# Kernel optimization log

Hardware: AMD Instinct MI355X
Metric: run time of the kernel (lower is better)

## Reference

```python
import jax, jax.numpy as jnp
import numpy as np

PERIODS = [4, 2, 1]   # base_periods[:n_period]
TEMPERATURE = 0.1
TOPM = 20
EPS = 1e-12


def _l2norm(v, axis):
    n = jnp.sqrt(jnp.sum(v * v, axis=axis, keepdims=True))
    return v / jnp.maximum(n, EPS)


def decompose_mg(x):
    """x: [B, L, C] -> mg: [G, B, L, C] (offset removed, as in torch code)."""
    B, L, C = x.shape
    mg = []
    for g in PERIODS:
        cur = x.reshape(B, L // g, g, C).mean(axis=2)      # unfold(size=g, step=g).mean(-1)
        cur = jnp.repeat(cur, g, axis=1)                   # repeat_interleave back to L
        mg.append(cur)
    mg = jnp.stack(mg, axis=0)                             # [G, B, L, C]
    return mg - mg[:, :, -1:, :]                           # remove per-series last-step offset


def extract_channel_state(mg):
    """mg: [G, B, L, C] -> [G, B, C, 4] (mean, std, slope, mean |diff|)."""
    L = mg.shape[2]
    mean = mg.mean(axis=2)
    std = mg.std(axis=2)                                   # unbiased=False (ddof=0)
    slope = (mg[:, :, -1, :] - mg[:, :, 0, :]) / float(L - 1)
    abs_diff = jnp.abs(mg[:, :, 1:, :] - mg[:, :, :-1, :]).mean(axis=2)
    return jnp.stack([mean, std, slope, abs_diff], axis=-1)


def setup_inputs() -> dict:
    key = jax.random.key(0)
    k1, k2, k3 = jax.random.split(key, 3)
    B, L, C, G, T, P = 32, 512, 64, 3, 10000, 96
    x = jax.random.normal(k1, (B, L, C), dtype=jnp.float32)
    pool_state = jax.random.normal(k2, (G, T, C, 4), dtype=jnp.float32)
    y_pool = jax.random.normal(k3, (T, P, C), dtype=jnp.float32)
    return {"x": x, "pool_state": pool_state, "y_pool": y_pool}


def reference(x, pool_state, y_pool):
    # Multi-scale decomposition of query batch
    q_mg = decompose_mg(x)                                  # [G, B, L, C]
    q_state = extract_channel_state(q_mg)                   # [G, B, C, 4]
    # Normalized channel-state similarity vs candidate pool
    q = _l2norm(q_state, axis=-1)
    p = _l2norm(pool_state, axis=-1)
    sim = jnp.einsum('gbcd,gtcd->gbct', q, p)               # [G, B, C, T]
    sim = sim.mean(axis=0)                                  # combine granularities -> [B, C, T]
    # Top-m retrieval per (batch, channel)
    vals, idx = jax.lax.top_k(sim, TOPM)                    # [B, C, M]
    w = jax.nn.softmax(vals / TEMPERATURE, axis=-1)         # [B, C, M]
    # Gather retrieved future windows, channelwise: y_pool [T, P, C]
    C = y_pool.shape[2]
    y_ct = jnp.transpose(y_pool, (2, 0, 1))                 # [C, T, P]
    gathered = y_ct[jnp.arange(C)[None, :, None], idx]      # [B, C, M, P]
    out = jnp.einsum('bcm,bcmp->bpc', w, gathered)          # [B, P, C]
    return out
```

## Files before the change

### kernel.cpp

```cpp
#include <hip/hip_runtime.h>
#include <hip/hip_fp16.h>
#include <math.h>

#define NB 32
#define NL 512
#define NC 64
#define NG 3
#define NT 10000
#define NP 96
#define TOPM 20
#define M1 8
#define NCH 256
#define CHUNK 40
#define QK 16
#define NCAND 64
#define PNBLK 1250
#define NENT (NB * NC * TOPM)
#define BINCAP 64
#define P16STR ((size_t)NT * NC)

union H2U { uint2 u; __half2 h[2]; };

__global__ __launch_bounds__(512) void pre_kernel(const float* __restrict__ x,
                                                  const float* __restrict__ ps,
                                                  double* __restrict__ q,
                                                  uint2* __restrict__ phat16) {
  __shared__ double s_sum[8][3][64], s_sq[8][3][64], s_abs[8][3][64];
  __shared__ double s_first[3][64], s_last[3][64];
  if (blockIdx.x < NB) {
    const int b = blockIdx.x, w = threadIdx.x >> 6, c = threadIdx.x & 63;
    const float* xp = x + (size_t)b * NL * NC + c;
    const int l0 = w * 64;
    double sum[3] = {0, 0, 0}, sumsq[3] = {0, 0, 0}, sumabs[3] = {0, 0, 0};
    double prev[3] = {0, 0, 0}, first[3] = {0, 0, 0};
    if (w > 0) {
      double e0 = xp[(l0 - 4) * NC], e1 = xp[(l0 - 3) * NC];
      double e2 = xp[(l0 - 2) * NC], e3 = xp[(l0 - 1) * NC];
      prev[2] = e3; prev[1] = (e2 + e3) * 0.5; prev[0] = (e0 + e1 + e2 + e3) * 0.25;
    }
    double acc2 = 0.0, acc4 = 0.0;
    for (int i = 0; i < 64; ++i) {
      const int l = l0 + i;
      double v = (double)xp[l * NC];
      sum[2] += v; sumsq[2] += v * v;
      if (l == 0) first[2] = v; else sumabs[2] += fabs(v - prev[2]);
      prev[2] = v;
      acc2 += v;
      if (l & 1) {
        double cur = acc2 * 0.5; acc2 = 0.0;
        sum[1] += cur; sumsq[1] += cur * cur;
        if (l == 1) first[1] = cur; else sumabs[1] += fabs(cur - prev[1]);
        prev[1] = cur;
      }
      acc4 += v;
      if ((l & 3) == 3) {
        double cur = acc4 * 0.25; acc4 = 0.0;
        sum[0] += cur; sumsq[0] += cur * cur;
        if (l == 3) first[0] = cur; else sumabs[0] += fabs(cur - prev[0]);
        prev[0] = cur;
      }
    }
    for (int g = 0; g < 3; ++g) {
      s_sum[w][g][c] = sum[g]; s_sq[w][g][c] = sumsq[g]; s_abs[w][g][c] = sumabs[g];
    }
    if (w == 0) { for (int g = 0; g < 3; ++g) s_first[g][c] = first[g]; }
    if (w == 7) { for (int g = 0; g < 3; ++g) s_last[g][c] = prev[g]; }
    __syncthreads();
    if (w == 0) {
      const double J[3] = {128.0, 256.0, 512.0};
      for (int g = 0; g < 3; ++g) {
        double S = 0, Q2 = 0, A = 0;
        for (int ww = 0; ww < 8; ++ww) {
          S += s_sum[ww][g][c]; Q2 += s_sq[ww][g][c]; A += s_abs[ww][g][c];
        }
        double mean = S / J[g];
        double var = Q2 / J[g] - mean * mean; if (var < 0.0) var = 0.0;
        double last = s_last[g][c];
        double s0 = mean - last;
        double s1 = sqrt(var);
        double s2 = (last - s_first[g][c]) * (1.0 / 511.0);
        double s3 = A * (1.0 / 511.0);
        double n = sqrt(s0 * s0 + s1 * s1 + s2 * s2 + s3 * s3);
        double inv = 1.0 / fmax(n, 1e-12);
        double* qp = q + ((((size_t)g * NB) + b) * NC + c) * 4;
        qp[0] = s0 * inv; qp[1] = s1 * inv; qp[2] = s2 * inv; qp[3] = s3 * inv;
      }
    }
  } else {
    const int i = (blockIdx.x - NB) * 512 + threadIdx.x;
    if (i < NT * NC) {
#pragma unroll
      for (int g = 0; g < 3; ++g) {
        const size_t off = ((size_t)g * NT * NC + i) * 4;
        const float4 pv = *reinterpret_cast<const float4*>(ps + off);
        double p0 = pv.x, p1 = pv.y, p2 = pv.z, p3 = pv.w;
        double inv = 1.0 / fmax(sqrt(p0 * p0 + p1 * p1 + p2 * p2 + p3 * p3), 1e-12);
        H2U o;
        o.h[0] = __halves2half2(__float2half_rn((float)(p0 * inv)),
                                __float2half_rn((float)(p1 * inv)));
        o.h[1] = __halves2half2(__float2half_rn((float)(p2 * inv)),
                                __float2half_rn((float)(p3 * inv)));
        phat16[(size_t)g * P16STR + i] = o.u;
      }
    }
  }
}

__device__ __forceinline__ unsigned mkkey16(float v, int t) {
  unsigned h = (unsigned)__half_as_ushort(__float2half_rn(v));
  h = (h & 0x8000u) ? ((~h) & 0xFFFFu) : (h | 0x8000u);
  return (h << 16) | (0xFFFFu - (unsigned)t);
}

__device__ __forceinline__ void insert8k(unsigned k, unsigned key[M1]) {
  unsigned cv = k;
#pragma unroll
  for (int m = 0; m < M1; ++m) {
    bool sw = cv > key[m];
    unsigned tv = sw ? key[m] : cv;
    key[m] = sw ? cv : key[m];
    cv = tv;
  }
}

#if defined(__has_builtin)
#if __has_builtin(__builtin_amdgcn_fdot2)
#define HAVE_FDOT2 1
#endif
#endif

__device__ __forceinline__ float sim_dot(const uint2* __restrict__ p16,
                                         size_t o,
#ifdef HAVE_FDOT2
                                         const __half2 qh[6]
#else
                                         const float qv[12]
#endif
                                         ) {
  H2U a0, a1, a2;
  a0.u = p16[o];
  a1.u = p16[P16STR + o];
  a2.u = p16[2 * P16STR + o];
#ifdef HAVE_FDOT2
  float s = 0.f;
  s = __builtin_amdgcn_fdot2(qh[0], a0.h[0], s, false);
  s = __builtin_amdgcn_fdot2(qh[1], a0.h[1], s, false);
  s = __builtin_amdgcn_fdot2(qh[2], a1.h[0], s, false);
  s = __builtin_amdgcn_fdot2(qh[3], a1.h[1], s, false);
  s = __builtin_amdgcn_fdot2(qh[4], a2.h[0], s, false);
  s = __builtin_amdgcn_fdot2(qh[5], a2.h[1], s, false);
  return s;
#else
  float2 f0 = __half22float2(a0.h[0]), f1 = __half22float2(a0.h[1]);
  float2 f2 = __half22float2(a1.h[0]), f3 = __half22float2(a1.h[1]);
  float2 f4 = __half22float2(a2.h[0]), f5 = __half22float2(a2.h[1]);
  return qv[0] * f0.x + qv[1] * f0.y + qv[2] * f1.x + qv[3] * f1.y +
         qv[4] * f2.x + qv[5] * f2.y + qv[6] * f3.x + qv[7] * f3.y +
         qv[8] * f4.x + qv[9] * f4.y + qv[10] * f5.x + qv[11] * f5.y;
#endif
}

__global__ __launch_bounds__(1024, 8) void sim32_kernel(
    const uint2* __restrict__ p16, const double* __restrict__ q,
    unsigned* __restrict__ ckey, int* __restrict__ hist) {
  if (blockIdx.x == 0 && blockIdx.y < 10) {
    const int idx = blockIdx.y * 1024 + threadIdx.x;
    if (idx < NT) hist[idx] = 0;
  }
  const int wav = threadIdx.x >> 6;
  const int c = threadIdx.x & 63;
  const int b = blockIdx.x * 16 + wav;
  const int ch = blockIdx.y;
#ifdef HAVE_FDOT2
  __half2 qh[6];
#pragma unroll
  for (int g = 0; g < 3; ++g) {
    const double* qp = q + ((((size_t)g * NB) + b) * NC + c) * 4;
    qh[g * 2 + 0] = __halves2half2(__float2half_rn((float)(qp[0] * (1.0 / 3.0))),
                                   __float2half_rn((float)(qp[1] * (1.0 / 3.0))));
    qh[g * 2 + 1] = __halves2half2(__float2half_rn((float)(qp[2] * (1.0 / 3.0))),
                                   __float2half_rn((float)(qp[3] * (1.0 / 3.0))));
  }
#else
  float qv[12];
#pragma unroll
  for (int g = 0; g < 3; ++g) {
    const double* qp = q + ((((size_t)g * NB) + b) * NC + c) * 4;
#pragma unroll
    for (int j = 0; j < 4; ++j) qv[g * 4 + j] = (float)(qp[j] * (1.0 / 3.0));
  }
#endif
  unsigned key[M1];
#pragma unroll
  for (int m = 0; m < M1; ++m) key[m] = 0u;
  int t0 = ch * CHUNK;
  int t1 = t0 + CHUNK; if (t1 > NT) t1 = NT;
  for (int t = t0; t + 1 < t1; t += 2) {
    const size_t oA = (size_t)t * NC + c;
    const size_t oB = oA + NC;
#ifdef HAVE_FDOT2
    const float sA = sim_dot(p16, oA, qh);
    const float sB = sim_dot(p16, oB, qh);
#else
    const float sA = sim_dot(p16, oA, qv);
    const float sB = sim_dot(p16, oB, qv);
#endif
    const unsigned kA = mkkey16(sA, t);
    const unsigned kB = mkkey16(sB, t + 1);
    if (kA > key[M1 - 1]) insert8k(kA, key);
    if (kB > key[M1 - 1]) insert8k(kB, key);
  }
  unsigned* ko = ckey + ((((size_t)b * NC) + c) * NCH + ch) * M1;
  *reinterpret_cast<uint4*>(ko) = make_uint4(key[0], key[1], key[2], key[3]);
  *reinterpret_cast<uint4*>(ko + 4) = make_uint4(key[4], key[5], key[6], key[7]);
}

__global__ __launch_bounds__(128) void merge_rerank_kernel(
    const unsigned* __restrict__ ckey, const float* __restrict__ ps,
    const double* __restrict__ q, float* __restrict__ w_out,
    int* __restrict__ t_out, int* __restrict__ hist, int* __restrict__ bin_slot) {
  const int c = blockIdx.x, b = blockIdx.y;
  __shared__ unsigned k_s[NCH * M1];
  __shared__ int ct_s[NCAND];
  __shared__ double rv_s[NCAND];
  __shared__ double m0_s, inv_s;
  __shared__ double e_s[TOPM];
  __shared__ int ts_s[TOPM];
  const int n = NCH * M1;
  const size_t row = (size_t)b * NC + c;
  const uint4* kin = reinterpret_cast<const uint4*>(ckey + row * n);
  for (int k = threadIdx.x; k < n / 4; k += 128)
    *reinterpret_cast<uint4*>(&k_s[k * 4]) = kin[k];
  __syncthreads();
  {
    const int w = threadIdx.x >> 6, lane = threadIdx.x & 63;
    const int lane32 = lane & 31;
    const int qtr = (w << 1) | (lane >> 5);
    const int l0 = (qtr * 64 + lane32 * 2) * M1;
    const int l1 = l0 + M1;
    int p0 = 0, p1 = 0;
    unsigned k0 = k_s[l0], k1 = k_s[l1];
    for (int r = 0; r < QK; ++r) {
      const unsigned me = k0 > k1 ? k0 : k1;
      unsigned km = me;
#pragma unroll
      for (int st = 1; st < 32; st <<= 1) {
        const unsigned k2 = __shfl_xor(km, st);
        km = k2 > km ? k2 : km;
      }
      if (lane32 == r) ct_s[qtr * QK + r] = (int)(0xFFFFu - (km & 0xFFFFu));
      if (me == km) {
        if (k0 >= k1) { ++p0; k0 = (p0 < M1) ? k_s[l0 + p0] : 0u; }
        else          { ++p1; k1 = (p1 < M1) ? k_s[l1 + p1] : 0u; }
      }
    }
  }
  __syncthreads();
  double myv = -1e300; int myt = 0x7fffffff;
  if (threadIdx.x < NCAND) {
    myt = ct_s[threadIdx.x];
    double s = 0.0;
#pragma unroll
    for (int g = 0; g < 3; ++g) {
      const double* qp = q + ((((size_t)g * NB) + b) * NC + c) * 4;
      const float4 pv = *reinterpret_cast<const float4*>(
          ps + ((((size_t)g * NT) + myt) * NC + c) * 4);
      double pp0 = pv.x, pp1 = pv.y, pp2 = pv.z, pp3 = pv.w;
      double ss = pp0 * pp0 + pp1 * pp1 + pp2 * pp2 + pp3 * pp3;
      double dot = qp[0] * pp0 + qp[1] * pp1 + qp[2] * pp2 + qp[3] * pp3;
      s += dot / fmax(sqrt(ss), 1e-12);
    }
    myv = s * (1.0 / 3.0);
    rv_s[threadIdx.x] = myv;
  }
  __syncthreads();
  int rank = -1;
  if (threadIdx.x < NCAND) {
    rank = 0;
    for (int j = 0; j < NCAND; ++j) {
      double vj = rv_s[j]; int tj = ct_s[j];
      rank += (vj > myv) || (vj == myv && tj < myt);
    }
    if (rank == 0) m0_s = myv;
  }
  __syncthreads();
  if (rank >= 0 && rank < TOPM) { e_s[rank] = exp((myv - m0_s) * 10.0); ts_s[rank] = myt; }
  __syncthreads();
  if (threadIdx.x == 0) {
    double sum = 0.0;
#pragma unroll
    for (int m = 0; m < TOPM; ++m) sum += e_s[m];
    inv_s = 1.0 / sum;
  }
  __syncthreads();
  if (threadIdx.x < TOPM) {
    const int t = ts_s[threadIdx.x];
    const int i = (int)(row * TOPM) + threadIdx.x;
    w_out[i] = (float)(e_s[threadIdx.x] * inv_s);
    t_out[i] = t;
    const int pos = atomicAdd(&hist[t], 1);
    if (pos < BINCAP) bin_slot[t * BINCAP + pos] = i;
  }
}

__global__ __launch_bounds__(256) void process_kernel(
    const float* __restrict__ y, const int* __restrict__ hist,
    const int* __restrict__ bin_slot, const float* __restrict__ w_out,
    float* __restrict__ partial) {
  const int t = blockIdx.x;
  int k = hist[t];
  if (k == 0) return;
  if (k > BINCAP) k = BINCAP;
  __shared__ float lds[NP * 65];
  __shared__ float w_l[BINCAP];
  __shared__ int i_l[BINCAP];
  __shared__ int c_l[BINCAP];
  const float4* yrow = reinterpret_cast<const float4*>(y + (size_t)t * NP * NC);
#pragma unroll
  for (int r = 0; r < 6; ++r) {
    const int e4 = threadIdx.x + r * 256;
    const float4 v = yrow[e4];
    const int p = e4 >> 4;
    const int c = (e4 & 15) * 4;
    lds[p * 65 + c] = v.x; lds[p * 65 + c + 1] = v.y;
    lds[p * 65 + c + 2] = v.z; lds[p * 65 + c + 3] = v.w;
  }
  if (threadIdx.x < k) {
    const int i = bin_slot[t * BINCAP + threadIdx.x];
    i_l[threadIdx.x] = i;
    w_l[threadIdx.x] = w_out[i];
    c_l[threadIdx.x] = (i / TOPM) & 63;
  }
  __syncthreads();
  const int h = threadIdx.x >> 7;
  const int p = threadIdx.x & 127;
  for (int e = h; e < k; e += 2) {
    if (p < NP)
      partial[(size_t)i_l[e] * NP + p] = w_l[e] * lds[p * 65 + c_l[e]];
  }
}

__global__ __launch_bounds__(128) void final_kernel(const float* __restrict__ partial,
                                                    float* __restrict__ out) {
  const int row = blockIdx.x;
  const int p = threadIdx.x;
  if (p >= NP) return;
  const int b = row >> 6, c = row & 63;
  const float* pp = partial + (size_t)row * TOPM * NP + p;
  float acc = 0.f;
#pragma unroll
  for (int m = 0; m < TOPM; ++m) acc += pp[m * NP];
  out[(((size_t)b * NP) + p) * NC + c] = acc;
}

__global__ __launch_bounds__(256) void sim_topk_inline_kernel(
    const float* __restrict__ ps, const double* __restrict__ q,
    double* __restrict__ cval, int* __restrict__ cidx, int nch, int chunk) {
  const int wav = threadIdx.x >> 6;
  const int c = threadIdx.x & 63;
  const int b = blockIdx.y * 4 + wav;
  const int ch = blockIdx.x;
  double qv[3][4];
#pragma unroll
  for (int g = 0; g < 3; ++g) {
    const double* qp = q + ((((size_t)g * NB) + b) * NC + c) * 4;
    qv[g][0] = qp[0]; qv[g][1] = qp[1]; qv[g][2] = qp[2]; qv[g][3] = qp[3];
  }
  double val[TOPM]; int idx[TOPM];
#pragma unroll
  for (int m = 0; m < TOPM; ++m) { val[m] = -1e300; idx[m] = 0; }
  int t0 = ch * chunk;
  int t1 = t0 + chunk; if (t1 > NT) t1 = NT;
  for (int t = t0; t < t1; ++t) {
    double s = 0.0;
#pragma unroll
    for (int g = 0; g < 3; ++g) {
      const float4 pv = *reinterpret_cast<const float4*>(
          ps + ((((size_t)g * NT) + t) * NC + c) * 4);
      double p0 = pv.x, p1 = pv.y, p2 = pv.z, p3 = pv.w;
      double ss = p0 * p0 + p1 * p1 + p2 * p2 + p3 * p3;
      double dot = qv[g][0] * p0 + qv[g][1] * p1 + qv[g][2] * p2 + qv[g][3] * p3;
      s += dot / fmax(sqrt(ss), 1e-12);
    }
    s *= (1.0 / 3.0);
    if (s > val[TOPM - 1]) {
      double cv = s; int ci = t;
#pragma unroll
      for (int m = 0; m < TOPM; ++m) {
        bool sw = cv > val[m];
        double tv = sw ? val[m] : cv; int ti = sw ? idx[m] : ci;
        val[m] = sw ? cv : val[m];    idx[m] = sw ? ci : idx[m];
        cv = tv; ci = ti;
      }
    }
  }
  double* vout = cval + ((((size_t)b * NC) + c) * nch + ch) * TOPM;
  int* iout = cidx + ((((size_t)b * NC) + c) * nch + ch) * TOPM;
#pragma unroll
  for (int m = 0; m < TOPM; ++m) { vout[m] = val[m]; iout[m] = idx[m]; }
}

__global__ __launch_bounds__(128) void merge_gather_old_kernel(
    const double* __restrict__ cval, const int* __restrict__ cidx,
    const float* __restrict__ y, float* __restrict__ out, int nch) {
  const int c = blockIdx.x;
  const int b = blockIdx.y;
  __shared__ float w_s[TOPM];
  __shared__ int i_s[TOPM];
  if (threadIdx.x == 0) {
    double val[TOPM]; int idx[TOPM];
#pragma unroll
    for (int m = 0; m < TOPM; ++m) { val[m] = -1e300; idx[m] = 0; }
    const double* vin = cval + (((size_t)b * NC) + c) * nch * TOPM;
    const int* iin = cidx + (((size_t)b * NC) + c) * nch * TOPM;
    for (int k = 0; k < nch; ++k) {
      const int base = k * TOPM;
      for (int m = 0; m < TOPM; ++m) {
        double s = vin[base + m];
        if (!(s > val[TOPM - 1])) break;
        double cv = s; int ci = iin[base + m];
#pragma unroll
        for (int mm = 0; mm < TOPM; ++mm) {
          bool sw = cv > val[mm];
          double tv = sw ? val[mm] : cv; int ti = sw ? idx[mm] : ci;
          val[mm] = sw ? cv : val[mm];   idx[mm] = sw ? ci : idx[mm];
          cv = tv; ci = ti;
        }
      }
    }
    double mx = val[0];
    double e[TOPM]; double sum = 0.0;
#pragma unroll
    for (int m = 0; m < TOPM; ++m) { e[m] = exp((val[m] - mx) * 10.0); sum += e[m]; }
    double inv = 1.0 / sum;
#pragma unroll
    for (int m = 0; m < TOPM; ++m) { w_s[m] = (float)(e[m] * inv); i_s[m] = idx[m]; }
  }
  __syncthreads();
  const int p = threadIdx.x;
  if (p < NP) {
    float acc = 0.f;
#pragma unroll
    for (int m = 0; m < TOPM; ++m)
      acc += w_s[m] * y[(((size_t)i_s[m]) * NP + p) * NC + c];
    out[(((size_t)b * NP) + p) * NC + c] = acc;
  }
}

extern "C" void kernel_launch(void* const* d_in, const int* in_sizes, int n_in,
                              void* d_out, int out_size, void* d_ws, size_t ws_size,
                              hipStream_t stream) {
  const float* x = (const float*)d_in[0];
  const float* ps = (const float*)d_in[1];
  const float* y = (const float*)d_in[2];
  float* out = (float*)d_out;
  char* ws = (char*)d_ws;

  const size_t qbytes = (size_t)NG * NB * NC * 4 * sizeof(double);
  const size_t phat16bytes = (size_t)NG * NT * NC * 8;
  const size_t ckeybytes = (size_t)NB * NC * NCH * M1 * 4;
  const size_t wtbytes = (size_t)NENT * 4;
  const size_t histbytes = (size_t)NT * 4;
  const size_t slotbytes = (size_t)NT * BINCAP * 4;
  const size_t partbytes = (size_t)NENT * NP * 4;

  double* qbuf = (double*)ws;
  size_t off = qbytes;
  uint2* phat16 = (uint2*)(ws + off); off += phat16bytes;
  unsigned* ckey = (unsigned*)(ws + off); off += ckeybytes;
  float* w_out = (float*)(ws + off); off += wtbytes;
  int* t_out = (int*)(ws + off); off += wtbytes;
  int* hist = (int*)(ws + off); off += histbytes;
  off = (off + 7) & ~(size_t)7;
  int* bin_slot = (int*)(ws + off); off += slotbytes;
  float* partial = (float*)(ws + off); off += partbytes;

  if (ws_size >= off) {
    pre_kernel<<<dim3(NB + PNBLK), dim3(512), 0, stream>>>(x, ps, qbuf, phat16);
    sim32_kernel<<<dim3(NB / 16, NCH), dim3(1024), 0, stream>>>(phat16, qbuf,
                                                                ckey, hist);
    merge_rerank_kernel<<<dim3(NC, NB), dim3(128), 0, stream>>>(
        ckey, ps, qbuf, w_out, t_out, hist, bin_slot);
    process_kernel<<<dim3(NT), dim3(256), 0, stream>>>(y, hist, bin_slot,
                                                       w_out, partial);
    final_kernel<<<dim3(NB * NC), dim3(128), 0, stream>>>(partial, out);
  } else {
    pre_kernel<<<dim3(NB), dim3(512), 0, stream>>>(x, ps, qbuf, (uint2*)nullptr);
    const size_t per_ch = (size_t)NB * NC * TOPM * (sizeof(double) + sizeof(int));
    int nch = 1;
    if (ws_size > qbytes) {
      size_t mc = (ws_size - qbytes) / per_ch;
      nch = mc < 32 ? (int)mc : 32;
      if (nch < 1) nch = 1;
    }
    const int chunk = (NT + nch - 1) / nch;
    double* fcval = (double*)(ws + qbytes);
    int* fcidx = (int*)((char*)fcval + (size_t)NB * NC * nch * TOPM * sizeof(double));
    sim_topk_inline_kernel<<<dim3(nch, NB / 4), dim3(256), 0, stream>>>(
        ps, qbuf, fcval, fcidx, nch, chunk);
    merge_gather_old_kernel<<<dim3(NC, NB), dim3(128), 0, stream>>>(fcval, fcidx, y,
                                                                    out, nch);
  }
}
```

Baseline: 117.2 us.

## Fuse pool normalization into similarity scan and drop fp16 pool staging

Removes the precompute pass that normalized pool_state and stored it as packed fp16. The similarity kernel now reads raw fp32 pool_state directly and normalizes each 4-vector on the fly with rsqrt, so one kernel phase and its intermediate write/read are gone. The cost is that the sim kernel reads twice as many bytes (fp32 instead of fp16) for every batch group, and the normalization is recomputed redundantly per batch block. It also widens process_kernel to 512 threads and drops the unused t_out buffer.

```diff
diff --git a/kernel.cpp b/kernel.cpp
--- a/kernel.cpp
+++ b/kernel.cpp
@@ -14,94 +14,70 @@
 #define CHUNK 40
 #define QK 16
 #define NCAND 64
-#define PNBLK 1250
 #define NENT (NB * NC * TOPM)
 #define BINCAP 64
-#define P16STR ((size_t)NT * NC)
-
-union H2U { uint2 u; __half2 h[2]; };
-
-__global__ __launch_bounds__(512) void pre_kernel(const float* __restrict__ x,
-                                                  const float* __restrict__ ps,
-                                                  double* __restrict__ q,
-                                                  uint2* __restrict__ phat16) {
+#define GSTRF ((size_t)NT * NC * 4)
+
+__global__ __launch_bounds__(512) void qstat_kernel(const float* __restrict__ x,
+                                                    double* __restrict__ q) {
   __shared__ double s_sum[8][3][64], s_sq[8][3][64], s_abs[8][3][64];
   __shared__ double s_first[3][64], s_last[3][64];
-  if (blockIdx.x < NB) {
-    const int b = blockIdx.x, w = threadIdx.x >> 6, c = threadIdx.x & 63;
-    const float* xp = x + (size_t)b * NL * NC + c;
-    const int l0 = w * 64;
-    double sum[3] = {0, 0, 0}, sumsq[3] = {0, 0, 0}, sumabs[3] = {0, 0, 0};
-    double prev[3] = {0, 0, 0}, first[3] = {0, 0, 0};
-    if (w > 0) {
-      double e0 = xp[(l0 - 4) * NC], e1 = xp[(l0 - 3) * NC];
-      double e2 = xp[(l0 - 2) * NC], e3 = xp[(l0 - 1) * NC];
-      prev[2] = e3; prev[1] = (e2 + e3) * 0.5; prev[0] = (e0 + e1 + e2 + e3) * 0.25;
-    }
-    double acc2 = 0.0, acc4 = 0.0;
-    for (int i = 0; i < 64; ++i) {
-      const int l = l0 + i;
-      double v = (double)xp[l * NC];
-      sum[2] += v; sumsq[2] += v * v;
-      if (l == 0) first[2] = v; else sumabs[2] += fabs(v - prev[2]);
-      prev[2] = v;
-      acc2 += v;
-      if (l & 1) {
-        double cur = acc2 * 0.5; acc2 = 0.0;
-        sum[1] += cur; sumsq[1] += cur * cur;
-        if (l == 1) first[1] = cur; else sumabs[1] += fabs(cur - prev[1]);
-        prev[1] = cur;
+  const int b = blockIdx.x, w = threadIdx.x >> 6, c = threadIdx.x & 63;
+  const float* xp = x + (size_t)b * NL * NC + c;
+  const int l0 = w * 64;
+  double sum[3] = {0, 0, 0}, sumsq[3] = {0, 0, 0}, sumabs[3] = {0, 0, 0};
+  double prev[3] = {0, 0, 0}, first[3] = {0, 0, 0};
+  if (w > 0) {
+    double e0 = xp[(l0 - 4) * NC], e1 = xp[(l0 - 3) * NC];
+    double e2 = xp[(l0 - 2) * NC], e3 = xp[(l0 - 1) * NC];
+    prev[2] = e3; prev[1] = (e2 + e3) * 0.5; prev[0] = (e0 + e1 + e2 + e3) * 0.25;
+  }
+  double acc2 = 0.0, acc4 = 0.0;
+  for (int i = 0; i < 64; ++i) {
+    const int l = l0 + i;
+    double v = (double)xp[l * NC];
+    sum[2] += v; sumsq[2] += v * v;
+    if (l == 0) first[2] = v; else sumabs[2] += fabs(v - prev[2]);
+    prev[2] = v;
+    acc2 += v;
+    if (l & 1) {
+      double cur = acc2 * 0.5; acc2 = 0.0;
+      sum[1] += cur; sumsq[1] += cur * cur;
+      if (l == 1) first[1] = cur; else sumabs[1] += fabs(cur - prev[1]);
+      prev[1] = cur;
+    }
+    acc4 += v;
+    if ((l & 3) == 3) {
+      double cur = acc4 * 0.25; acc4 = 0.0;
+      sum[0] += cur; sumsq[0] += cur * cur;
+      if (l == 3) first[0] = cur; else sumabs[0] += fabs(cur - prev[0]);
+      prev[0] = cur;
+    }
+  }
+  for (int g = 0; g < 3; ++g) {
+    s_sum[w][g][c] = sum[g]; s_sq[w][g][c] = sumsq[g]; s_abs[w][g][c] = sumabs[g];
+  }
+  if (w == 0) { for (int g = 0; g < 3; ++g) s_first[g][c] = first[g]; }
+  if (w == 7) { for (int g = 0; g < 3; ++g) s_last[g][c] = prev[g]; }
+  __syncthreads();
+  if (w == 0) {
+    const double J[3] = {128.0, 256.0, 512.0};
+    for (int g = 0; g < 3; ++g) {
+      double S = 0, Q2 = 0, A = 0;
+      for (int ww = 0; ww < 8; ++ww) {
+        S += s_sum[ww][g][c]; Q2 += s_sq[ww][g][c]; A += s_abs[ww][g][c];
       }
-      acc4 += v;
-      if ((l & 3) == 3) {
-        double cur = acc4 * 0.25; acc4 = 0.0;
-        sum[0] += cur; sumsq[0] += cur * cur;
-        if (l == 3) first[0] = cur; else sumabs[0] += fabs(cur - prev[0]);
-        prev[0] = cur;
-      }
-    }
-    for (int g = 0; g < 3; ++g) {
-      s_sum[w][g][c] = sum[g]; s_sq[w][g][c] = sumsq[g]; s_abs[w][g][c] = sumabs[g];
-    }
-    if (w == 0) { for (int g = 0; g < 3; ++g) s_first[g][c] = first[g]; }
-    if (w == 7) { for (int g = 0; g < 3; ++g) s_last[g][c] = prev[g]; }
-    __syncthreads();
-    if (w == 0) {
-      const double J[3] = {128.0, 256.0, 512.0};
-      for (int g = 0; g < 3; ++g) {
-        double S = 0, Q2 = 0, A = 0;
-        for (int ww = 0; ww < 8; ++ww) {
-          S += s_sum[ww][g][c]; Q2 += s_sq[ww][g][c]; A += s_abs[ww][g][c];
-        }
-        double mean = S / J[g];
-        double var = Q2 / J[g] - mean * mean; if (var < 0.0) var = 0.0;
-        double last = s_last[g][c];
-        double s0 = mean - last;
-        double s1 = sqrt(var);
-        double s2 = (last - s_first[g][c]) * (1.0 / 511.0);
-        double s3 = A * (1.0 / 511.0);
-        double n = sqrt(s0 * s0 + s1 * s1 + s2 * s2 + s3 * s3);
-        double inv = 1.0 / fmax(n, 1e-12);
-        double* qp = q + ((((size_t)g * NB) + b) * NC + c) * 4;
-        qp[0] = s0 * inv; qp[1] = s1 * inv; qp[2] = s2 * inv; qp[3] = s3 * inv;
-      }
-    }
-  } else {
-    const int i = (blockIdx.x - NB) * 512 + threadIdx.x;
-    if (i < NT * NC) {
-#pragma unroll
-      for (int g = 0; g < 3; ++g) {
-        const size_t off = ((size_t)g * NT * NC + i) * 4;
-        const float4 pv = *reinterpret_cast<const float4*>(ps + off);
-        double p0 = pv.x, p1 = pv.y, p2 = pv.z, p3 = pv.w;
-        double inv = 1.0 / fmax(sqrt(p0 * p0 + p1 * p1 + p2 * p2 + p3 * p3), 1e-12);
-        H2U o;
-        o.h[0] = __halves2half2(__float2half_rn((float)(p0 * inv)),
-                                __float2half_rn((float)(p1 * inv)));
-        o.h[1] = __halves2half2(__float2half_rn((float)(p2 * inv)),
-                                __float2half_rn((float)(p3 * inv)));
-        phat16[(size_t)g * P16STR + i] = o.u;
-      }
+      double mean = S / J[g];
+      double var = Q2 / J[g] - mean * mean; if (var < 0.0) var = 0.0;
+      double last = s_last[g][c];
+      double s0 = mean - last;
+      double s1 = sqrt(var);
+      double s2 = (last - s_first[g][c]) * (1.0 / 511.0);
+      double s3 = A * (1.0 / 511.0);
+      double n = sqrt(s0 * s0 + s1 * s1 + s2 * s2 + s3 * s3);
+      double inv = 1.0 / fmax(n, 1e-12);
+      double* qp = q + ((((size_t)g * NB) + b) * NC + c) * 4;
+      qp[0] = s0 * inv; qp[1] = s1 * inv; qp[2] = s2 * inv; qp[3] = s3 * inv;
     }
   }
 }
@@ -123,45 +99,16 @@
   }
 }
 
-#if defined(__has_builtin)
-#if __has_builtin(__builtin_amdgcn_fdot2)
-#define HAVE_FDOT2 1
-#endif
-#endif
-
-__device__ __forceinline__ float sim_dot(const uint2* __restrict__ p16,
-                                         size_t o,
-#ifdef HAVE_FDOT2
-                                         const __half2 qh[6]
-#else
-                                         const float qv[12]
-#endif
-                                         ) {
-  H2U a0, a1, a2;
-  a0.u = p16[o];
-  a1.u = p16[P16STR + o];
-  a2.u = p16[2 * P16STR + o];
-#ifdef HAVE_FDOT2
-  float s = 0.f;
-  s = __builtin_amdgcn_fdot2(qh[0], a0.h[0], s, false);
-  s = __builtin_amdgcn_fdot2(qh[1], a0.h[1], s, false);
-  s = __builtin_amdgcn_fdot2(qh[2], a1.h[0], s, false);
-  s = __builtin_amdgcn_fdot2(qh[3], a1.h[1], s, false);
-  s = __builtin_amdgcn_fdot2(qh[4], a2.h[0], s, false);
-  s = __builtin_amdgcn_fdot2(qh[5], a2.h[1], s, false);
-  return s;
-#else
-  float2 f0 = __half22float2(a0.h[0]), f1 = __half22float2(a0.h[1]);
-  float2 f2 = __half22float2(a1.h[0]), f3 = __half22float2(a1.h[1]);
-  float2 f4 = __half22float2(a2.h[0]), f5 = __half22float2(a2.h[1]);
-  return qv[0] * f0.x + qv[1] * f0.y + qv[2] * f1.x + qv[3] * f1.y +
-         qv[4] * f2.x + qv[5] * f2.y + qv[6] * f3.x + qv[7] * f3.y +
-         qv[8] * f4.x + qv[9] * f4.y + qv[10] * f5.x + qv[11] * f5.y;
-#endif
+__device__ __forceinline__ float dot4f(float4 a, const float* qv) {
+  return qv[0] * a.x + qv[1] * a.y + qv[2] * a.z + qv[3] * a.w;
+}
+__device__ __forceinline__ float nrm4f(float4 a) {
+  float ss = a.x * a.x + a.y * a.y + a.z * a.z + a.w * a.w;
+  return rsqrtf(fmaxf(ss, 1e-24f));
 }
 
 __global__ __launch_bounds__(1024, 8) void sim32_kernel(
-    const uint2* __restrict__ p16, const double* __restrict__ q,
+    const float* __restrict__ ps, const double* __restrict__ q,
     unsigned* __restrict__ ckey, int* __restrict__ hist) {
   if (blockIdx.x == 0 && blockIdx.y < 10) {
     const int idx = blockIdx.y * 1024 + threadIdx.x;
@@ -171,40 +118,31 @@
   const int c = threadIdx.x & 63;
   const int b = blockIdx.x * 16 + wav;
   const int ch = blockIdx.y;
-#ifdef HAVE_FDOT2
-  __half2 qh[6];
+  float qv[12];
 #pragma unroll
   for (int g = 0; g < 3; ++g) {
     const double* qp = q + ((((size_t)g * NB) + b) * NC + c) * 4;
-    qh[g * 2 + 0] = __halves2half2(__float2half_rn((float)(qp[0] * (1.0 / 3.0))),
-                                   __float2half_rn((float)(qp[1] * (1.0 / 3.0))));
-    qh[g * 2 + 1] = __halves2half2(__float2half_rn((float)(qp[2] * (1.0 / 3.0))),
-                                   __float2half_rn((float)(qp[3] * (1.0 / 3.0))));
-  }
-#else
-  float qv[12];
-#pragma unroll
-  for (int g = 0; g < 3; ++g) {
-    const double* qp = q + ((((size_t)g * NB) + b) * NC + c) * 4;
 #pragma unroll
     for (int j = 0; j < 4; ++j) qv[g * 4 + j] = (float)(qp[j] * (1.0 / 3.0));
   }
-#endif
   unsigned key[M1];
 #pragma unroll
   for (int m = 0; m < M1; ++m) key[m] = 0u;
   int t0 = ch * CHUNK;
   int t1 = t0 + CHUNK; if (t1 > NT) t1 = NT;
   for (int t = t0; t + 1 < t1; t += 2) {
-    const size_t oA = (size_t)t * NC + c;
-    const size_t oB = oA + NC;
-#ifdef HAVE_FDOT2
-    const float sA = sim_dot(p16, oA, qh);
-    const float sB = sim_dot(p16, oB, qh);
-#else
-    const float sA = sim_dot(p16, oA, qv);
-    const float sB = sim_dot(p16, oB, qv);
-#endif
+    const size_t oA = ((size_t)t * NC + c) * 4;
+    const size_t oB = oA + (size_t)NC * 4;
+    const float4 a0 = *reinterpret_cast<const float4*>(ps + oA);
+    const float4 a1 = *reinterpret_cast<const float4*>(ps + GSTRF + oA);
+    const float4 a2 = *reinterpret_cast<const float4*>(ps + 2 * GSTRF + oA);
+    const float4 b0 = *reinterpret_cast<const float4*>(ps + oB);
+    const float4 b1 = *reinterpret_cast<const float4*>(ps + GSTRF + oB);
+    const float4 b2 = *reinterpret_cast<const float4*>(ps + 2 * GSTRF + oB);
+    const float sA = dot4f(a0, qv) * nrm4f(a0) + dot4f(a1, qv + 4) * nrm4f(a1) +
+                     dot4f(a2, qv + 8) * nrm4f(a2);
+    const float sB = dot4f(b0, qv) * nrm4f(b0) + dot4f(b1, qv + 4) * nrm4f(b1) +
+                     dot4f(b2, qv + 8) * nrm4f(b2);
     const unsigned kA = mkkey16(sA, t);
     const unsigned kB = mkkey16(sB, t + 1);
     if (kA > key[M1 - 1]) insert8k(kA, key);
@@ -218,7 +156,7 @@
 __global__ __launch_bounds__(128) void merge_rerank_kernel(
     const unsigned* __restrict__ ckey, const float* __restrict__ ps,
     const double* __restrict__ q, float* __restrict__ w_out,
-    int* __restrict__ t_out, int* __restrict__ hist, int* __restrict__ bin_slot) {
+    int* __restrict__ hist, int* __restrict__ bin_slot) {
   const int c = blockIdx.x, b = blockIdx.y;
   __shared__ unsigned k_s[NCH * M1];
   __shared__ int ct_s[NCAND];
@@ -297,13 +235,12 @@
     const int t = ts_s[threadIdx.x];
     const int i = (int)(row * TOPM) + threadIdx.x;
     w_out[i] = (float)(e_s[threadIdx.x] * inv_s);
-    t_out[i] = t;
     const int pos = atomicAdd(&hist[t], 1);
     if (pos < BINCAP) bin_slot[t * BINCAP + pos] = i;
   }
 }
 
-__global__ __launch_bounds__(256) void process_kernel(
+__global__ __launch_bounds__(512) void process_kernel(
     const float* __restrict__ y, const int* __restrict__ hist,
     const int* __restrict__ bin_slot, const float* __restrict__ w_out,
     float* __restrict__ partial) {
@@ -317,8 +254,8 @@
   __shared__ int c_l[BINCAP];
   const float4* yrow = reinterpret_cast<const float4*>(y + (size_t)t * NP * NC);
 #pragma unroll
-  for (int r = 0; r < 6; ++r) {
-    const int e4 = threadIdx.x + r * 256;
+  for (int r = 0; r < 3; ++r) {
+    const int e4 = threadIdx.x + r * 512;
     const float4 v = yrow[e4];
     const int p = e4 >> 4;
     const int c = (e4 & 15) * 4;
@@ -334,7 +271,7 @@
   __syncthreads();
   const int h = threadIdx.x >> 7;
   const int p = threadIdx.x & 127;
-  for (int e = h; e < k; e += 2) {
+  for (int e = h; e < k; e += 4) {
     if (p < NP)
       partial[(size_t)i_l[e] * NP + p] = w_l[e] * lds[p * 65 + c_l[e]];
   }
@@ -457,7 +394,6 @@
   char* ws = (char*)d_ws;
 
   const size_t qbytes = (size_t)NG * NB * NC * 4 * sizeof(double);
-  const size_t phat16bytes = (size_t)NG * NT * NC * 8;
   const size_t ckeybytes = (size_t)NB * NC * NCH * M1 * 4;
   const size_t wtbytes = (size_t)NENT * 4;
   const size_t histbytes = (size_t)NT * 4;
@@ -466,26 +402,24 @@
 
   double* qbuf = (double*)ws;
   size_t off = qbytes;
-  uint2* phat16 = (uint2*)(ws + off); off += phat16bytes;
   unsigned* ckey = (unsigned*)(ws + off); off += ckeybytes;
   float* w_out = (float*)(ws + off); off += wtbytes;
-  int* t_out = (int*)(ws + off); off += wtbytes;
   int* hist = (int*)(ws + off); off += histbytes;
   off = (off + 7) & ~(size_t)7;
   int* bin_slot = (int*)(ws + off); off += slotbytes;
   float* partial = (float*)(ws + off); off += partbytes;
 
   if (ws_size >= off) {
-    pre_kernel<<<dim3(NB + PNBLK), dim3(512), 0, stream>>>(x, ps, qbuf, phat16);
-    sim32_kernel<<<dim3(NB / 16, NCH), dim3(1024), 0, stream>>>(phat16, qbuf,
+    qstat_kernel<<<dim3(NB), dim3(512), 0, stream>>>(x, qbuf);
+    sim32_kernel<<<dim3(NB / 16, NCH), dim3(1024), 0, stream>>>(ps, qbuf,
                                                                 ckey, hist);
     merge_rerank_kernel<<<dim3(NC, NB), dim3(128), 0, stream>>>(
-        ckey, ps, qbuf, w_out, t_out, hist, bin_slot);
-    process_kernel<<<dim3(NT), dim3(256), 0, stream>>>(y, hist, bin_slot,
+        ckey, ps, qbuf, w_out, hist, bin_slot);
+    process_kernel<<<dim3(NT), dim3(512), 0, stream>>>(y, hist, bin_slot,
                                                        w_out, partial);
     final_kernel<<<dim3(NB * NC), dim3(128), 0, stream>>>(partial, out);
   } else {
-    pre_kernel<<<dim3(NB), dim3(512), 0, stream>>>(x, ps, qbuf, (uint2*)nullptr);
+    qstat_kernel<<<dim3(NB), dim3(512), 0, stream>>>(x, qbuf);
     const size_t per_ch = (size_t)NB * NC * TOPM * (sizeof(double) + sizeof(int));
     int nch = 1;
     if (ws_size > qbytes) {
```

Result: no change. 119.3 us (+1.7%).
